# Kernel tuning notes

Hardware: AMD Instinct MI355X
Metric: run time of the kernel (lower is better)

Reference implementation:

```python
import jax, jax.numpy as jnp
import numpy as np

N_SLICES = 2  # init kwarg n_slices


def affine_grid_3d(theta, D, H, W):
    """torch.nn.functional.affine_grid for 5D output, align_corners=False.
    theta: [B,3,4]; returns grid [B,D,H,W,3] with last dim (x,y,z) ~ (W,H,D)."""
    xs = (jnp.arange(W, dtype=theta.dtype) + 0.5) * (2.0 / W) - 1.0
    ys = (jnp.arange(H, dtype=theta.dtype) + 0.5) * (2.0 / H) - 1.0
    zs = (jnp.arange(D, dtype=theta.dtype) + 0.5) * (2.0 / D) - 1.0
    zz, yy, xx = jnp.meshgrid(zs, ys, xs, indexing='ij')
    base = jnp.stack([xx, yy, zz, jnp.ones_like(xx)], axis=-1)  # [D,H,W,4]
    return jnp.einsum('bij,dhwj->bdhwi', theta, base)  # [B,D,H,W,3]


def grid_sample_3d_zeros(vol, grid):
    """torch.nn.functional.grid_sample, mode='bilinear' (trilinear for 5D),
    padding_mode='zeros', align_corners=False.
    vol: [B,C,D,H,W]; grid: [B,D,H,W,3] normalized xyz coords."""
    B, C, D, H, W = vol.shape
    ix = ((grid[..., 0] + 1.0) * W - 1.0) * 0.5
    iy = ((grid[..., 1] + 1.0) * H - 1.0) * 0.5
    iz = ((grid[..., 2] + 1.0) * D - 1.0) * 0.5
    ix0 = jnp.floor(ix); iy0 = jnp.floor(iy); iz0 = jnp.floor(iz)
    fx = ix - ix0; fy = iy - iy0; fz = iz - iz0

    def gather(v, z, y, x):  # v: [C,D,H,W], idx: [D,H,W] -> [C,D,H,W]
        return v[:, z, y, x]

    out = jnp.zeros((B, C, D, H, W), vol.dtype)
    for dz in (0, 1):
        for dy in (0, 1):
            for dx in (0, 1):
                xi = ix0 + dx; yi = iy0 + dy; zi = iz0 + dz
                w = (jnp.where(dx, fx, 1.0 - fx)
                     * jnp.where(dy, fy, 1.0 - fy)
                     * jnp.where(dz, fz, 1.0 - fz))
                valid = ((xi >= 0) & (xi < W) & (yi >= 0) & (yi < H)
                         & (zi >= 0) & (zi < D))
                xc = jnp.clip(xi, 0, W - 1).astype(jnp.int32)
                yc = jnp.clip(yi, 0, H - 1).astype(jnp.int32)
                zc = jnp.clip(zi, 0, D - 1).astype(jnp.int32)
                vals = jax.vmap(gather)(vol, zc, yc, xc)  # [B,C,D,H,W]
                out = out + vals * (w * valid)[:, None]
    return out


def skip_connector(x, b_grid_affines):
    B, C, SPAT, _ = x.shape
    # zero volume with the 2D slice stack placed at the central W-plane
    vol = jnp.zeros((B, C, SPAT, SPAT, SPAT), x.dtype).at[..., SPAT // 2].set(x)
    chunks = jnp.split(vol, N_SLICES, axis=1)
    outs = []
    for i in range(N_SLICES):
        aff = b_grid_affines[i].astype(jnp.float32)  # [B,4,4]
        # get_zooms: column norms of rotation block
        zooms = jnp.sqrt((aff[:, :3, :3] ** 2).sum(axis=1))  # [B,3]
        # rescale_rot_components_with_diag(aff, 1/zooms) == aff @ diag(1/zx,1/zy,1/zz,1)
        scale = jnp.concatenate([1.0 / zooms, jnp.ones((aff.shape[0], 1), aff.dtype)], axis=1)
        aff = aff * scale[:, None, :]
        theta = jnp.linalg.inv(aff)[:, :3, :]  # [B,3,4]
        grid = affine_grid_3d(theta, SPAT, SPAT, SPAT)
        outs.append(grid_sample_3d_zeros(chunks[i], grid))
    return jnp.concatenate(outs, axis=1)  # [B,C,SPAT,SPAT,SPAT]


def setup_inputs() -> dict:
    key = jax.random.key(0)
    k1, k2 = jax.random.split(key)
    B, C, SPAT = 2, 32, 96
    x = jax.random.normal(k1, (B, C, SPAT, SPAT), dtype=jnp.float32)
    # near-identity invertible homogeneous affines for the two views (SA, HLA)
    noise = 0.1 * jax.random.normal(k2, (2, B, 4, 4), dtype=jnp.float32)
    aff = jnp.eye(4, dtype=jnp.float32)[None, None] + noise
    aff = aff.at[..., 3, :].set(jnp.array([0.0, 0.0, 0.0, 1.0], dtype=jnp.float32))
    return {"x": x, "b_grid_affines": aff}


def reference(x, b_grid_affines):
    return skip_connector(x, b_grid_affines)
```

## Files before the change

### kernel.cpp

```cpp
#include <hip/hip_runtime.h>
#include <math.h>

#define SPAT  96
#define IMG   (SPAT*SPAT)
#define PLANE (SPAT*SPAT*SPAT)

__device__ inline void invert4(const float m[16], float inv[16]) {
    inv[0]  =  m[5]*m[10]*m[15] - m[5]*m[11]*m[14] - m[9]*m[6]*m[15] + m[9]*m[7]*m[14] + m[13]*m[6]*m[11] - m[13]*m[7]*m[10];
    inv[4]  = -m[4]*m[10]*m[15] + m[4]*m[11]*m[14] + m[8]*m[6]*m[15] - m[8]*m[7]*m[14] - m[12]*m[6]*m[11] + m[12]*m[7]*m[10];
    inv[8]  =  m[4]*m[9]*m[15]  - m[4]*m[11]*m[13] - m[8]*m[5]*m[15] + m[8]*m[7]*m[13] + m[12]*m[5]*m[11] - m[12]*m[7]*m[9];
    inv[12] = -m[4]*m[9]*m[14]  + m[4]*m[10]*m[13] + m[8]*m[5]*m[14] - m[8]*m[6]*m[13] - m[12]*m[5]*m[10] + m[12]*m[6]*m[9];
    inv[1]  = -m[1]*m[10]*m[15] + m[1]*m[11]*m[14] + m[9]*m[2]*m[15] - m[9]*m[3]*m[14] - m[13]*m[2]*m[11] + m[13]*m[3]*m[10];
    inv[5]  =  m[0]*m[10]*m[15] - m[0]*m[11]*m[14] - m[8]*m[2]*m[15] + m[8]*m[3]*m[14] + m[12]*m[2]*m[11] - m[12]*m[3]*m[10];
    inv[9]  = -m[0]*m[9]*m[15]  + m[0]*m[11]*m[13] + m[8]*m[1]*m[15] - m[8]*m[3]*m[13] - m[12]*m[1]*m[11] + m[12]*m[3]*m[9];
    inv[13] =  m[0]*m[9]*m[14]  - m[0]*m[10]*m[13] - m[8]*m[1]*m[14] + m[8]*m[2]*m[13] + m[12]*m[1]*m[10] - m[12]*m[2]*m[9];
    inv[2]  =  m[1]*m[6]*m[15]  - m[1]*m[7]*m[14]  - m[5]*m[2]*m[15] + m[5]*m[3]*m[14] + m[13]*m[2]*m[7]  - m[13]*m[3]*m[6];
    inv[6]  = -m[0]*m[6]*m[15]  + m[0]*m[7]*m[14]  + m[4]*m[2]*m[15] - m[4]*m[3]*m[14] - m[12]*m[2]*m[7]  + m[12]*m[3]*m[6];
    inv[10] =  m[0]*m[5]*m[15]  - m[0]*m[7]*m[13]  - m[4]*m[1]*m[15] + m[4]*m[3]*m[13] + m[12]*m[1]*m[7]  - m[12]*m[3]*m[5];
    inv[14] = -m[0]*m[5]*m[14]  + m[0]*m[6]*m[13]  + m[4]*m[1]*m[14] - m[4]*m[2]*m[13] - m[12]*m[1]*m[6]  + m[12]*m[2]*m[5];
    inv[3]  = -m[1]*m[6]*m[11]  + m[1]*m[7]*m[10]  + m[5]*m[2]*m[11] - m[5]*m[3]*m[10] - m[9]*m[2]*m[7]   + m[9]*m[3]*m[6];
    inv[7]  =  m[0]*m[6]*m[11]  - m[0]*m[7]*m[10]  - m[4]*m[2]*m[11] + m[4]*m[3]*m[10] + m[8]*m[2]*m[7]   - m[8]*m[3]*m[6];
    inv[11] = -m[0]*m[5]*m[11]  + m[0]*m[7]*m[9]   + m[4]*m[1]*m[11] - m[4]*m[3]*m[9]  - m[8]*m[1]*m[7]   + m[8]*m[3]*m[5];
    inv[15] =  m[0]*m[5]*m[10]  - m[0]*m[6]*m[9]   - m[4]*m[1]*m[10] + m[4]*m[2]*m[9]  + m[8]*m[1]*m[6]   - m[8]*m[2]*m[5];
    float det  = m[0]*inv[0] + m[1]*inv[4] + m[2]*inv[8] + m[3]*inv[12];
    float rdet = 1.0f / det;
    for (int i = 0; i < 16; ++i) inv[i] *= rdet;
}

__global__ __launch_bounds__(256) void fused2_kernel(
        const float* __restrict__ xin,
        const float* __restrict__ aff_in,
        float4* __restrict__ out) {
    __shared__ float Ms[12];
    const int d  = blockIdx.x;
    const int cc = blockIdx.y;
    const int b  = cc >> 5;
    const int s  = (cc >> 4) & 1;
    const int sb = s * 2 + b;

    if (threadIdx.x == 0) {
        float A[16];
        #pragma unroll
        for (int i = 0; i < 16; ++i) A[i] = aff_in[sb * 16 + i];
        #pragma unroll
        for (int j = 0; j < 3; ++j) {
            float z = sqrtf(A[0*4+j]*A[0*4+j] + A[1*4+j]*A[1*4+j] + A[2*4+j]*A[2*4+j]);
            float rz = 1.0f / z;
            #pragma unroll
            for (int i = 0; i < 4; ++i) A[i*4+j] *= rz;
        }
        float inv[16];
        invert4(A, inv);
        #pragma unroll
        for (int r = 0; r < 3; ++r) {
            float T0 = inv[r*4+0], T1 = inv[r*4+1], T2 = inv[r*4+2], T3 = inv[r*4+3];
            Ms[r*4+0] = T0;
            Ms[r*4+1] = T1;
            Ms[r*4+2] = T2;
            Ms[r*4+3] = -47.5f * (T0 + T1 + T2) + 48.0f * T3 + 47.5f;
        }
    }

    float4* op = out + ((size_t)cc * (PLANE / 4) + (size_t)d * (IMG / 4));
    const float4 z4 = make_float4(0.f, 0.f, 0.f, 0.f);
    #pragma unroll
    for (int it = 0; it < 9; ++it)
        op[(int)threadIdx.x + 256 * it] = z4;

    __syncthreads();

    const int h = (int)threadIdx.x;
    if (h >= SPAT) return;

    const float Mxw = Ms[0], Mxh = Ms[1], Mxd = Ms[2],  Mx0 = Ms[3];
    const float Myw = Ms[4], Myh = Ms[5], Myd = Ms[6],  My0 = Ms[7];
    const float Mzw = Ms[8], Mzh = Ms[9], Mzd = Ms[10], Mz0 = Ms[11];

    const float fh = (float)h, fd = (float)d;
    const float bx = Mxh * fh + Mxd * fd + Mx0;

    int wlo, whi;
    if (fabsf(Mxw) > 1e-6f) {
        float rMxw = 1.0f / Mxw;
        float w1 = (47.0f - bx) * rMxw;
        float w2 = (49.0f - bx) * rMxw;
        float wmin = fminf(w1, w2), wmax = fmaxf(w1, w2);
        wlo = max((int)ceilf(wmin), 0);
        whi = min((int)floorf(wmax), SPAT - 1);
    } else {
        bool in = fabsf(bx - 48.0f) < 1.0f;
        wlo = in ? 0 : 1;
        whi = in ? SPAT - 1 : 0;
    }
    if (wlo > whi) return;

    const float by = Myh * fh + Myd * fd + My0;
    const float bz = Mzh * fh + Mzd * fd + Mz0;
    const float* img = xin + (size_t)cc * IMG;

    const int qlo = wlo >> 2, qhi = whi >> 2;
    for (int q = qlo; q <= qhi; ++q) {
        float vv[4];
        #pragma unroll
        for (int j = 0; j < 4; ++j) {
            float fw = (float)(4 * q + j);
            float ix = Mxw * fw + bx;
            float wx = 1.0f - fabsf(ix - 48.0f);
            float r = 0.0f;
            if (wx > 0.0f) {
                float iy = Myw * fw + by;
                float iz = Mzw * fw + bz;
                float yf = floorf(iy), zf = floorf(iz);
                float fy = iy - yf,    fz = iz - zf;
                int y0 = (int)yf, z0 = (int)zf;
                bool vy0 = (y0 >= 0)  & (y0 <  SPAT);
                bool vy1 = (y0 >= -1) & (y0 <  SPAT - 1);
                bool vz0 = (z0 >= 0)  & (z0 <  SPAT);
                bool vz1 = (z0 >= -1) & (z0 <  SPAT - 1);
                int y0c = min(max(y0, 0),     SPAT - 1);
                int y1c = min(max(y0 + 1, 0), SPAT - 1);
                int z0c = min(max(z0, 0),     SPAT - 1);
                int z1c = min(max(z0 + 1, 0), SPAT - 1);
                float wy0 = 1.0f - fy, wy1 = fy;
                float wz0 = 1.0f - fz, wz1 = fz;
                float w00 = wx * wz0 * wy0 * ((vz0 & vy0) ? 1.0f : 0.0f);
                float w01 = wx * wz0 * wy1 * ((vz0 & vy1) ? 1.0f : 0.0f);
                float w10 = wx * wz1 * wy0 * ((vz1 & vy0) ? 1.0f : 0.0f);
                float w11 = wx * wz1 * wy1 * ((vz1 & vy1) ? 1.0f : 0.0f);
                r = w00 * img[z0c * SPAT + y0c] + w01 * img[z0c * SPAT + y1c]
                  + w10 * img[z1c * SPAT + y0c] + w11 * img[z1c * SPAT + y1c];
            }
            vv[j] = r;
        }
        op[h * 24 + q] = make_float4(vv[0], vv[1], vv[2], vv[3]);
    }
}

extern "C" void kernel_launch(void* const* d_in, const int* in_sizes, int n_in,
                              void* d_out, int out_size, void* d_ws, size_t ws_size,
                              hipStream_t stream) {
    const float* x   = (const float*)d_in[0];
    const float* aff = (const float*)d_in[1];
    float* out = (float*)d_out;

    dim3 grid(SPAT, 64);
    fused2_kernel<<<grid, 256, 0, stream>>>(x, aff, (float4*)out);
}
```

Baseline: 223.2 us.

## Stage input slice in LDS, write each output once with nontemporal stores

```diff
diff --git a/kernel.cpp b/kernel.cpp
--- a/kernel.cpp
+++ b/kernel.cpp
@@ -4,6 +4,10 @@
 #define SPAT  96
 #define IMG   (SPAT*SPAT)
 #define PLANE (SPAT*SPAT*SPAT)
+#define DPB   8
+#define NRI   (DPB*SPAT)
+
+typedef float f32x4 __attribute__((ext_vector_type(4)));
 
 __device__ inline void invert4(const float m[16], float inv[16]) {
     inv[0]  =  m[5]*m[10]*m[15] - m[5]*m[11]*m[14] - m[9]*m[6]*m[15] + m[9]*m[7]*m[14] + m[13]*m[6]*m[11] - m[13]*m[7]*m[10];
@@ -27,112 +31,142 @@
     for (int i = 0; i < 16; ++i) inv[i] *= rdet;
 }
 
-__global__ __launch_bounds__(256) void fused2_kernel(
+__device__ inline void fold_affine(const float* __restrict__ aff_in, int sb,
+                                   float M[12]) {
+    float A[16];
+    #pragma unroll
+    for (int i = 0; i < 16; ++i) A[i] = aff_in[sb * 16 + i];
+    #pragma unroll
+    for (int j = 0; j < 3; ++j) {
+        float z = sqrtf(A[0*4+j]*A[0*4+j] + A[1*4+j]*A[1*4+j] + A[2*4+j]*A[2*4+j]);
+        float rz = 1.0f / z;
+        #pragma unroll
+        for (int i = 0; i < 4; ++i) A[i*4+j] *= rz;
+    }
+    float inv[16];
+    invert4(A, inv);
+    #pragma unroll
+    for (int r = 0; r < 3; ++r) {
+        float T0 = inv[r*4+0], T1 = inv[r*4+1], T2 = inv[r*4+2], T3 = inv[r*4+3];
+        M[r*4+0] = T0;
+        M[r*4+1] = T1;
+        M[r*4+2] = T2;
+        M[r*4+3] = -47.5f * (T0 + T1 + T2) + 48.0f * T3 + 47.5f;
+    }
+}
+
+__global__ __launch_bounds__(256) void fused5_kernel(
         const float* __restrict__ xin,
         const float* __restrict__ aff_in,
-        float4* __restrict__ out) {
-    __shared__ float Ms[12];
-    const int d  = blockIdx.x;
-    const int cc = blockIdx.y;
-    const int b  = cc >> 5;
-    const int s  = (cc >> 4) & 1;
-    const int sb = s * 2 + b;
+        float* __restrict__ out) {
+    __shared__ float    simg[IMG];
+    __shared__ unsigned rinf[NRI];
+    const int tid  = (int)threadIdx.x;
+    const int cc   = blockIdx.x;
+    const int d0   = (int)blockIdx.y * DPB;
+    const int b    = cc >> 5;
+    const int s    = (cc >> 4) & 1;
+    const int sb   = s * 2 + b;
 
-    if (threadIdx.x == 0) {
-        float A[16];
-        #pragma unroll
-        for (int i = 0; i < 16; ++i) A[i] = aff_in[sb * 16 + i];
-        #pragma unroll
-        for (int j = 0; j < 3; ++j) {
-            float z = sqrtf(A[0*4+j]*A[0*4+j] + A[1*4+j]*A[1*4+j] + A[2*4+j]*A[2*4+j]);
-            float rz = 1.0f / z;
-            #pragma unroll
-            for (int i = 0; i < 4; ++i) A[i*4+j] *= rz;
+    float M[12];
+    fold_affine(aff_in, sb, M);
+    const float Mxw = M[0], Mxh = M[1], Mxd = M[2],  Mx0 = M[3];
+    const float Myw = M[4], Myh = M[5], Myd = M[6],  My0 = M[7];
+    const float Mzw = M[8], Mzh = M[9], Mzd = M[10], Mz0 = M[11];
+
+    const f32x4* ip = reinterpret_cast<const f32x4*>(xin + (size_t)cc * IMG);
+    f32x4* sp = reinterpret_cast<f32x4*>(simg);
+    #pragma unroll
+    for (int i = 0; i < IMG / 4 / 256; ++i)
+        sp[tid + 256 * i] = ip[tid + 256 * i];
+
+    for (int r = tid; r < NRI; r += 256) {
+        const int dp = r / SPAT;
+        const int h  = r - dp * SPAT;
+        const float fh = (float)h, fd = (float)(d0 + dp);
+        const float bx = Mxh * fh + Mxd * fd + Mx0;
+        int wlo, whi;
+        if (fabsf(Mxw) > 1e-6f) {
+            float rMxw = 1.0f / Mxw;
+            float w1 = (47.0f - bx) * rMxw;
+            float w2 = (49.0f - bx) * rMxw;
+            float wmin = fminf(w1, w2), wmax = fmaxf(w1, w2);
+            wlo = max((int)ceilf(wmin), 0);
+            whi = min((int)floorf(wmax), SPAT - 1);
+        } else {
+            bool in = fabsf(bx - 48.0f) < 1.0f;
+            wlo = in ? 0 : 1;
+            whi = in ? SPAT - 1 : 0;
         }
-        float inv[16];
-        invert4(A, inv);
-        #pragma unroll
-        for (int r = 0; r < 3; ++r) {
-            float T0 = inv[r*4+0], T1 = inv[r*4+1], T2 = inv[r*4+2], T3 = inv[r*4+3];
-            Ms[r*4+0] = T0;
-            Ms[r*4+1] = T1;
-            Ms[r*4+2] = T2;
-            Ms[r*4+3] = -47.5f * (T0 + T1 + T2) + 48.0f * T3 + 47.5f;
-        }
+        rinf[r] = (wlo > whi) ? 0xFFu
+                : ((unsigned)(wlo >> 2) | ((unsigned)(whi >> 2) << 8));
     }
-
-    float4* op = out + ((size_t)cc * (PLANE / 4) + (size_t)d * (IMG / 4));
-    const float4 z4 = make_float4(0.f, 0.f, 0.f, 0.f);
-    #pragma unroll
-    for (int it = 0; it < 9; ++it)
-        op[(int)threadIdx.x + 256 * it] = z4;
 
     __syncthreads();
 
-    const int h = (int)threadIdx.x;
-    if (h >= SPAT) return;
+    int hh[9], qq[9];
+    #pragma unroll
+    for (int it = 0; it < 9; ++it) {
+        const int tl = tid + 256 * it;
+        hh[it] = tl / 24;
+        qq[it] = tl - hh[it] * 24;
+    }
 
-    const float Mxw = Ms[0], Mxh = Ms[1], Mxd = Ms[2],  Mx0 = Ms[3];
-    const float Myw = Ms[4], Myh = Ms[5], Myd = Ms[6],  My0 = Ms[7];
-    const float Mzw = Ms[8], Mzh = Ms[9], Mzd = Ms[10], Mz0 = Ms[11];
-
-    const float fh = (float)h, fd = (float)d;
-    const float bx = Mxh * fh + Mxd * fd + Mx0;
-
-    int wlo, whi;
-    if (fabsf(Mxw) > 1e-6f) {
-        float rMxw = 1.0f / Mxw;
-        float w1 = (47.0f - bx) * rMxw;
-        float w2 = (49.0f - bx) * rMxw;
-        float wmin = fminf(w1, w2), wmax = fmaxf(w1, w2);
-        wlo = max((int)ceilf(wmin), 0);
-        whi = min((int)floorf(wmax), SPAT - 1);
-    } else {
-        bool in = fabsf(bx - 48.0f) < 1.0f;
-        wlo = in ? 0 : 1;
-        whi = in ? SPAT - 1 : 0;
-    }
-    if (wlo > whi) return;
-
-    const float by = Myh * fh + Myd * fd + My0;
-    const float bz = Mzh * fh + Mzd * fd + Mz0;
-    const float* img = xin + (size_t)cc * IMG;
-
-    const int qlo = wlo >> 2, qhi = whi >> 2;
-    for (int q = qlo; q <= qhi; ++q) {
-        float vv[4];
+    for (int dp = 0; dp < DPB; ++dp) {
+        const float fd  = (float)(d0 + dp);
+        const float bxd = Mxd * fd + Mx0;
+        const float byd = Myd * fd + My0;
+        const float bzd = Mzd * fd + Mz0;
+        f32x4* op = reinterpret_cast<f32x4*>(out
+            + (size_t)cc * PLANE + (size_t)(d0 + dp) * IMG);
         #pragma unroll
-        for (int j = 0; j < 4; ++j) {
-            float fw = (float)(4 * q + j);
-            float ix = Mxw * fw + bx;
-            float wx = 1.0f - fabsf(ix - 48.0f);
-            float r = 0.0f;
-            if (wx > 0.0f) {
-                float iy = Myw * fw + by;
-                float iz = Mzw * fw + bz;
-                float yf = floorf(iy), zf = floorf(iz);
-                float fy = iy - yf,    fz = iz - zf;
-                int y0 = (int)yf, z0 = (int)zf;
-                bool vy0 = (y0 >= 0)  & (y0 <  SPAT);
-                bool vy1 = (y0 >= -1) & (y0 <  SPAT - 1);
-                bool vz0 = (z0 >= 0)  & (z0 <  SPAT);
-                bool vz1 = (z0 >= -1) & (z0 <  SPAT - 1);
-                int y0c = min(max(y0, 0),     SPAT - 1);
-                int y1c = min(max(y0 + 1, 0), SPAT - 1);
-                int z0c = min(max(z0, 0),     SPAT - 1);
-                int z1c = min(max(z0 + 1, 0), SPAT - 1);
-                float wy0 = 1.0f - fy, wy1 = fy;
-                float wz0 = 1.0f - fz, wz1 = fz;
-                float w00 = wx * wz0 * wy0 * ((vz0 & vy0) ? 1.0f : 0.0f);
-                float w01 = wx * wz0 * wy1 * ((vz0 & vy1) ? 1.0f : 0.0f);
-                float w10 = wx * wz1 * wy0 * ((vz1 & vy0) ? 1.0f : 0.0f);
-                float w11 = wx * wz1 * wy1 * ((vz1 & vy1) ? 1.0f : 0.0f);
-                r = w00 * img[z0c * SPAT + y0c] + w01 * img[z0c * SPAT + y1c]
-                  + w10 * img[z1c * SPAT + y0c] + w11 * img[z1c * SPAT + y1c];
+        for (int it = 0; it < 9; ++it) {
+            const int h = hh[it], q = qq[it];
+            const unsigned info = rinf[dp * SPAT + h];
+            const bool ins = ((unsigned)q >= (info & 0xFFu))
+                           & ((unsigned)q <= ((info >> 8) & 0xFFu));
+            f32x4 v = {0.f, 0.f, 0.f, 0.f};
+            if (ins) {
+                const float fh = (float)h;
+                const float bx = Mxh * fh + bxd;
+                const float by = Myh * fh + byd;
+                const float bz = Mzh * fh + bzd;
+                #pragma unroll
+                for (int j = 0; j < 4; ++j) {
+                    float fw = (float)(4 * q + j);
+                    float ix = Mxw * fw + bx;
+                    float wx = 1.0f - fabsf(ix - 48.0f);
+                    float r = 0.0f;
+                    if (wx > 0.0f) {
+                        float iy = Myw * fw + by;
+                        float iz = Mzw * fw + bz;
+                        float yf = floorf(iy), zf = floorf(iz);
+                        float fy = iy - yf,    fz = iz - zf;
+                        int y0 = (int)yf, z0 = (int)zf;
+                        bool vy0 = (y0 >= 0)  & (y0 <  SPAT);
+                        bool vy1 = (y0 >= -1) & (y0 <  SPAT - 1);
+                        bool vz0 = (z0 >= 0)  & (z0 <  SPAT);
+                        bool vz1 = (z0 >= -1) & (z0 <  SPAT - 1);
+                        int y0c = min(max(y0, 0),     SPAT - 1);
+                        int y1c = min(max(y0 + 1, 0), SPAT - 1);
+                        int z0c = min(max(z0, 0),     SPAT - 1);
+                        int z1c = min(max(z0 + 1, 0), SPAT - 1);
+                        float wy0 = 1.0f - fy, wy1 = fy;
+                        float wz0 = 1.0f - fz, wz1 = fz;
+                        float w00 = wx * wz0 * wy0 * ((vz0 & vy0) ? 1.0f : 0.0f);
+                        float w01 = wx * wz0 * wy1 * ((vz0 & vy1) ? 1.0f : 0.0f);
+                        float w10 = wx * wz1 * wy0 * ((vz1 & vy0) ? 1.0f : 0.0f);
+                        float w11 = wx * wz1 * wy1 * ((vz1 & vy1) ? 1.0f : 0.0f);
+                        r = w00 * simg[z0c * SPAT + y0c]
+                          + w01 * simg[z0c * SPAT + y1c]
+                          + w10 * simg[z1c * SPAT + y0c]
+                          + w11 * simg[z1c * SPAT + y1c];
+                    }
+                    v[j] = r;
+                }
             }
-            vv[j] = r;
+            __builtin_nontemporal_store(v, op + (tid + 256 * it));
         }
-        op[h * 24 + q] = make_float4(vv[0], vv[1], vv[2], vv[3]);
     }
 }
 
@@ -143,6 +177,6 @@
     const float* aff = (const float*)d_in[1];
     float* out = (float*)d_out;
 
-    dim3 grid(SPAT, 64);
-    fused2_kernel<<<grid, 256, 0, stream>>>(x, aff, (float4*)out);
+    dim3 grid(64, SPAT / DPB);
+    fused5_kernel<<<grid, 256, 0, stream>>>(x, aff, out);
 }
```

Result: slower. 282.4 us (+26.5%).
